# Kernel optimization log

Measured on AMD Instinct MI355X. Metric: run time of the kernel, lower is better.

Reference implementation:

```python
import jax, jax.numpy as jnp
import numpy as np

D_MODEL = 1024
HIDDEN = 4096
N_EXPERTS = 8
TOP_K = 2


def setup_inputs() -> dict:
    key = jax.random.key(0)
    ks = jax.random.split(key, 7)
    x = jax.random.normal(ks[0], (4, 2048, D_MODEL), dtype=jnp.float32)
    s = 0.02
    Wg = jax.random.normal(ks[1], (D_MODEL, N_EXPERTS), dtype=jnp.float32) * s
    bg = jnp.zeros((N_EXPERTS,), dtype=jnp.float32)
    W1 = jax.random.normal(ks[2], (N_EXPERTS, D_MODEL, HIDDEN), dtype=jnp.float32) * s
    b1 = jnp.zeros((N_EXPERTS, HIDDEN), dtype=jnp.float32)
    W2 = jax.random.normal(ks[3], (N_EXPERTS, HIDDEN, D_MODEL), dtype=jnp.float32) * s
    b2 = jnp.zeros((N_EXPERTS, D_MODEL), dtype=jnp.float32)
    return {"x": x, "Wg": Wg, "bg": bg, "W1": W1, "b1": b1, "W2": W2, "b2": b2}


def reference(x, Wg, bg, W1, b1, W2, b2):
    B, T, D = x.shape
    xf = x.reshape(-1, D)                      # (N, D)
    N = xf.shape[0]

    # --- top-k gate ---
    logits = xf @ Wg + bg                      # (N, E)
    all_probs = jax.nn.softmax(logits, axis=-1)
    topk_logits, topk_idx = jax.lax.top_k(logits, TOP_K)   # (N, k)
    topk_gates = jax.nn.softmax(topk_logits, axis=-1)      # (N, k), sums to 1

    # scatter gates into dense (N, E) masks (matches torch scatter_add_)
    rows = jnp.arange(N)[:, None]
    gate_mask = jnp.zeros((N, N_EXPERTS), dtype=xf.dtype).at[rows, topk_idx].add(topk_gates)
    dispatch_mask = jnp.zeros((N, N_EXPERTS), dtype=xf.dtype).at[rows, topk_idx].add(1.0)

    # --- experts: dense batched form; unselected tokens have gate 0 so math matches ---
    h = jnp.einsum('nd,edh->neh', xf, W1) + b1             # (N, E, H)
    h = jax.nn.relu(h)
    y = jnp.einsum('neh,ehd->ned', h, W2) + b2             # (N, E, D)
    out = jnp.einsum('ned,ne->nd', y, gate_mask)           # weighted combine
    outputs = out.reshape(B, T, D)

    # --- load-balance loss + metadata ---
    tokens_per_expert = (dispatch_mask > 0).sum(axis=0)
    assignment_fraction = gate_mask.sum(axis=0) / N
    expected_prob = all_probs.mean(axis=0)
    load_balance_loss = (expected_prob * assignment_fraction).sum() * N_EXPERTS

    return (outputs, load_balance_loss, tokens_per_expert, expected_prob, assignment_fraction)
```

## Files before the change

kernel.cpp:

```cpp
#include <hip/hip_runtime.h>
#include <stdint.h>

#define D_MODEL 1024
#define HID     4096
#define NE      8
#define NTOK    8192
#define NSLOT   (NTOK*2)
#define TM      128
#define MAX_RB  136
#define MPAD    (MAX_RB*TM)
#define HHALF   2048
#define GATE_BLOCKS 32

typedef unsigned short u16;
typedef __attribute__((ext_vector_type(8))) __bf16 bf16x8;
typedef __attribute__((ext_vector_type(4))) float  f32x4;

__device__ __forceinline__ u16 f2bu(float f){
  uint32_t u = __builtin_bit_cast(uint32_t, f);
  uint32_t r = (u + 0x7FFFu + ((u >> 16) & 1u)) >> 16;
  return (u16)r;
}

__device__ __forceinline__ void gload16(const u16* src, u16* lds){
  __builtin_amdgcn_global_load_lds((const __attribute__((address_space(1))) void*)src,
                                   (__attribute__((address_space(3))) void*)lds, 16, 0, 0);
}

__device__ __forceinline__ int xcd_swz(int w, int nwg){
  int q = nwg >> 3;
  return (w & 7) * q + (w >> 3);
}

__global__ __launch_bounds__(256) void xcvt_kernel(const float* __restrict__ x, u16* __restrict__ x16){
  size_t i = (size_t)blockIdx.x*256 + threadIdx.x;
  const float4* p = (const float4*)(x + i*8);
  float4 a = p[0], b = p[1];
  u16 o[8] = {f2bu(a.x),f2bu(a.y),f2bu(a.z),f2bu(a.w),f2bu(b.x),f2bu(b.y),f2bu(b.z),f2bu(b.w)};
  *(int4*)(x16 + i*8) = *(int4*)o;
}

__global__ __launch_bounds__(256) void transpose_cvt(const float* __restrict__ in,
                                                     u16* __restrict__ out, int R, int C)
{
  __shared__ float tile[32][33];
  int e = blockIdx.z;
  int r0 = blockIdx.y * 32, c0 = blockIdx.x * 32;
  const float* src = in + (size_t)e * R * C;
  u16* dst = out + (size_t)e * R * C;
  int tx = threadIdx.x, ty = threadIdx.y;
#pragma unroll
  for (int i = 0; i < 4; i++){
    int r = r0 + ty + i*8;
    tile[ty + i*8][tx] = src[(size_t)r * C + c0 + tx];
  }
  __syncthreads();
#pragma unroll
  for (int i = 0; i < 4; i++){
    int c = c0 + ty + i*8;
    dst[(size_t)c * R + r0 + tx] = f2bu(tile[tx][ty + i*8]);
  }
}

__global__ __launch_bounds__(256) void gate_kernel(
    const float* __restrict__ x, const float* __restrict__ Wg, const float* __restrict__ bg,
    int* __restrict__ topk, float* __restrict__ gates,
    float* __restrict__ part_probs, float* __restrict__ part_assign, int* __restrict__ part_cnt)
{
  __shared__ float sp[256][8];
  __shared__ float sa[256][8];
  __shared__ int   sc[256][8];
  int t = threadIdx.x;
  int n = blockIdx.x * 256 + t;
  float lg[8];
#pragma unroll
  for (int e = 0; e < 8; e++) lg[e] = bg[e];
  const float4* xr = (const float4*)(x + (size_t)n * D_MODEL);
  for (int j = 0; j < D_MODEL/4; j++){
    float4 v = xr[j];
    const float* wr = Wg + (size_t)j * 32;
#pragma unroll
    for (int e = 0; e < 8; e++)
      lg[e] += v.x*wr[e] + v.y*wr[8+e] + v.z*wr[16+e] + v.w*wr[24+e];
  }
  float m = lg[0];
#pragma unroll
  for (int e = 1; e < 8; e++) m = fmaxf(m, lg[e]);
  float p[8]; float s = 0.f;
#pragma unroll
  for (int e = 0; e < 8; e++){ p[e] = expf(lg[e]-m); s += p[e]; }
  float inv = 1.f / s;
  int bi = 0; float best = lg[0];
#pragma unroll
  for (int e = 1; e < 8; e++) if (lg[e] > best){ best = lg[e]; bi = e; }
  int bi2 = 0; float best2 = -3.0e38f;
#pragma unroll
  for (int e = 0; e < 8; e++) if (e != bi && lg[e] > best2){ best2 = lg[e]; bi2 = e; }
  float t1 = expf(best2 - best);
  float g0 = 1.f / (1.f + t1);
  float g1 = t1 / (1.f + t1);
  topk[2*n] = bi;  topk[2*n+1] = bi2;
  gates[2*n] = g0; gates[2*n+1] = g1;
#pragma unroll
  for (int e = 0; e < 8; e++){
    sp[t][e] = p[e] * inv;
    sa[t][e] = (e == bi) ? g0 : ((e == bi2) ? g1 : 0.f);
    sc[t][e] = (e == bi || e == bi2) ? 1 : 0;
  }
  __syncthreads();
  if (t < 8){
    float s2 = 0.f; for (int i = 0; i < 256; i++) s2 += sp[i][t];
    part_probs[blockIdx.x*8 + t] = s2;
  } else if (t < 16){
    int e = t - 8; float s2 = 0.f; for (int i = 0; i < 256; i++) s2 += sa[i][e];
    part_assign[blockIdx.x*8 + e] = s2;
  } else if (t < 24){
    int e = t - 16; int c = 0; for (int i = 0; i < 256; i++) c += sc[i][e];
    part_cnt[blockIdx.x*8 + e] = c;
  }
}

__global__ __launch_bounds__(256) void scan_kernel(const int* __restrict__ part_cnt,
                                                   int* __restrict__ counts,
                                                   int* __restrict__ padded_off,
                                                   int* __restrict__ cursor,
                                                   int* __restrict__ block_expert,
                                                   int* __restrict__ routed)
{
  __shared__ int off[NE+1];
  int t = threadIdx.x;
  if (t == 0){
    int o = 0; off[0] = 0;
    for (int e = 0; e < NE; e++){
      int c = 0;
      for (int b = 0; b < GATE_BLOCKS; b++) c += part_cnt[b*8 + e];
      counts[e] = c;
      o += ((c + TM - 1) / TM) * TM;
      off[e+1] = o;
    }
    for (int e = 0; e <= NE; e++) padded_off[e] = off[e];
  }
  __syncthreads();
  if (t < NE) cursor[t] = 0;
  for (int rb = t; rb < MAX_RB; rb += 256){
    int e = -1;
    int r = rb * TM;
    for (int j = 0; j < NE; j++)
      if (r >= off[j] && r < off[j+1]) e = j;
    block_expert[rb] = e;
  }
  for (int i = t; i < MPAD; i += 256) routed[i] = -1;
}

__global__ __launch_bounds__(256) void place_kernel(const int* __restrict__ topk,
                                                    const int* __restrict__ padded_off,
                                                    int* __restrict__ cursor,
                                                    int* __restrict__ routed)
{
  int s = blockIdx.x * 256 + threadIdx.x;
  int e = topk[s];
  int pos = padded_off[e] + atomicAdd(&cursor[e], 1);
  routed[pos] = s;
}

__global__ __launch_bounds__(256) void gemm1_kernel(
    const u16* __restrict__ x16, const u16* __restrict__ w1t, const float* __restrict__ b1,
    const int* __restrict__ routed, const int* __restrict__ block_expert,
    u16* __restrict__ h, int half)
{
  int l = xcd_swz(blockIdx.x, gridDim.x);
  int rb = l >> 4, cb = l & 15;
  int e = block_expert[rb];
  if (e < 0) return;
  __shared__ __align__(16) u16 Al[2][128][32];
  __shared__ __align__(16) u16 Bl[2][128][32];
  int t = threadIdx.x;
  int lane = t & 63, wid = t >> 6;

  int srow0 = wid*32 + (lane >> 2);
  int srow1 = srow0 + 16;
  int sch = (lane & 3) * 8;

  int slot0 = routed[rb*TM + srow0];
  int slot1 = routed[rb*TM + srow1];
  int tok0 = slot0 >= 0 ? (slot0 >> 1) : 0;
  int tok1 = slot1 >= 0 ? (slot1 >> 1) : 0;
  const u16* srcA0 = x16 + (size_t)tok0 * D_MODEL + sch;
  const u16* srcA1 = x16 + (size_t)tok1 * D_MODEL + sch;
  const u16* wb = w1t + ((size_t)e*HID + (size_t)half*HHALF + (size_t)cb*128) * D_MODEL + sch;
  const u16* srcB0 = wb + (size_t)srow0 * D_MODEL;
  const u16* srcB1 = wb + (size_t)srow1 * D_MODEL;

  int wr = wid >> 1, wc = wid & 1;
  int fr = lane & 15, fk = lane >> 4;
  f32x4 acc[4][4];
#pragma unroll
  for (int i = 0; i < 4; i++)
#pragma unroll
    for (int j = 0; j < 4; j++) acc[i][j] = (f32x4){0.f,0.f,0.f,0.f};

#define STAGE1(bi, kk) do{ \
    gload16(srcA0 + (kk), &Al[bi][wid*32][0]); \
    gload16(srcA1 + (kk), &Al[bi][wid*32+16][0]); \
    gload16(srcB0 + (kk), &Bl[bi][wid*32][0]); \
    gload16(srcB1 + (kk), &Bl[bi][wid*32+16][0]); } while(0)

#define COMPUTE1(bi) do{ \
    bf16x8 af[4], bf[4]; \
    _Pragma("unroll") \
    for (int mm = 0; mm < 4; mm++) af[mm] = *(const bf16x8*)(&Al[bi][wr*64 + mm*16 + fr][fk*8]); \
    _Pragma("unroll") \
    for (int nn = 0; nn < 4; nn++) bf[nn] = *(const bf16x8*)(&Bl[bi][wc*64 + nn*16 + fr][fk*8]); \
    _Pragma("unroll") \
    for (int mm = 0; mm < 4; mm++) \
      _Pragma("unroll") \
      for (int nn = 0; nn < 4; nn++) \
        acc[mm][nn] = __builtin_amdgcn_mfma_f32_16x16x32_bf16(af[mm], bf[nn], acc[mm][nn], 0, 0, 0); } while(0)

  STAGE1(0, 0);
  __syncthreads();
  for (int k = 0; k < D_MODEL; k += 64){
    STAGE1(1, k + 32);
    COMPUTE1(0);
    __syncthreads();
    if (k + 64 < D_MODEL) STAGE1(0, k + 64);
    COMPUTE1(1);
    __syncthreads();
  }

  int r4 = fk * 4;
#pragma unroll
  for (int nn = 0; nn < 4; nn++){
    int ct = wc*64 + nn*16 + fr;
    float bias = b1[(size_t)e*HID + (size_t)half*HHALF + cb*128 + ct];
#pragma unroll
    for (int mm = 0; mm < 4; mm++){
#pragma unroll
      for (int r = 0; r < 4; r++){
        int rt = wr*64 + mm*16 + r4 + r;
        float v = acc[mm][nn][r] + bias;
        v = v > 0.f ? v : 0.f;
        h[(size_t)(rb*TM + rt) * HHALF + cb*128 + ct] = f2bu(v);
      }
    }
  }
#undef STAGE1
#undef COMPUTE1
}

__global__ __launch_bounds__(256) void gemm2_kernel(
    const u16* __restrict__ h, const u16* __restrict__ w2t,
    const int* __restrict__ routed, const int* __restrict__ block_expert,
    const float* __restrict__ gates, float* __restrict__ y, int half)
{
  int l = xcd_swz(blockIdx.x, gridDim.x);
  int rb = l >> 3, cb = l & 7;
  int e = block_expert[rb];
  if (e < 0) return;
  __shared__ __align__(16) u16 Al[2][128][32];
  __shared__ __align__(16) u16 Bl[2][128][32];
  __shared__ int   rslot[128];
  __shared__ float rgate[128];
  int t = threadIdx.x;
  int lane = t & 63, wid = t >> 6;
  if (t < 128){
    int s = routed[rb*TM + t];
    rslot[t] = s;
    rgate[t] = (s >= 0) ? gates[s] : 0.f;
  }

  int srow0 = wid*32 + (lane >> 2);
  int srow1 = srow0 + 16;
  int sch = (lane & 3) * 8;
  const u16* srcA0 = h + (size_t)(rb*TM + srow0) * HHALF + sch;
  const u16* srcA1 = h + (size_t)(rb*TM + srow1) * HHALF + sch;
  const u16* wb = w2t + ((size_t)e*D_MODEL + (size_t)cb*128) * HID + (size_t)half*HHALF + sch;
  const u16* srcB0 = wb + (size_t)srow0 * HID;
  const u16* srcB1 = wb + (size_t)srow1 * HID;

  int wr = wid >> 1, wc = wid & 1;
  int fr = lane & 15, fk = lane >> 4;
  f32x4 acc[4][4];
#pragma unroll
  for (int i = 0; i < 4; i++)
#pragma unroll
    for (int j = 0; j < 4; j++) acc[i][j] = (f32x4){0.f,0.f,0.f,0.f};

#define STAGE2(bi, kk) do{ \
    gload16(srcA0 + (kk), &Al[bi][wid*32][0]); \
    gload16(srcA1 + (kk), &Al[bi][wid*32+16][0]); \
    gload16(srcB0 + (kk), &Bl[bi][wid*32][0]); \
    gload16(srcB1 + (kk), &Bl[bi][wid*32+16][0]); } while(0)

#define COMPUTE2(bi) do{ \
    bf16x8 af[4], bf[4]; \
    _Pragma("unroll") \
    for (int mm = 0; mm < 4; mm++) af[mm] = *(const bf16x8*)(&Al[bi][wr*64 + mm*16 + fr][fk*8]); \
    _Pragma("unroll") \
    for (int nn = 0; nn < 4; nn++) bf[nn] = *(const bf16x8*)(&Bl[bi][wc*64 + nn*16 + fr][fk*8]); \
    _Pragma("unroll") \
    for (int mm = 0; mm < 4; mm++) \
      _Pragma("unroll") \
      for (int nn = 0; nn < 4; nn++) \
        acc[mm][nn] = __builtin_amdgcn_mfma_f32_16x16x32_bf16(af[mm], bf[nn], acc[mm][nn], 0, 0, 0); } while(0)

  STAGE2(0, 0);
  __syncthreads();
  for (int k = 0; k < HHALF; k += 64){
    STAGE2(1, k + 32);
    COMPUTE2(0);
    __syncthreads();
    if (k + 64 < HHALF) STAGE2(0, k + 64);
    COMPUTE2(1);
    __syncthreads();
  }

  int r4 = fk * 4;
#pragma unroll
  for (int mm = 0; mm < 4; mm++){
#pragma unroll
    for (int r = 0; r < 4; r++){
      int rt = wr*64 + mm*16 + r4 + r;
      int slot = rslot[rt];
      if (slot < 0) continue;
      float g = rgate[rt];
#pragma unroll
      for (int nn = 0; nn < 4; nn++){
        int ct = wc*64 + nn*16 + fr;
        size_t idx = (size_t)slot * D_MODEL + cb*128 + ct;
        float val = g * acc[mm][nn][r];
        if (half == 0) y[idx] = val;
        else           y[idx] += val;
      }
    }
  }
#undef STAGE2
#undef COMPUTE2
}

__global__ __launch_bounds__(256) void combine_kernel(
    const float* __restrict__ y, const int* __restrict__ topk, const float* __restrict__ gates,
    const float* __restrict__ b2, float* __restrict__ out)
{
  int i = blockIdx.x * 256 + threadIdx.x;
  int n = i >> 8;
  int d = (i & 255) * 4;
  float4 a  = *(const float4*)(y + (size_t)(2*n)   * D_MODEL + d);
  float4 b  = *(const float4*)(y + (size_t)(2*n+1) * D_MODEL + d);
  int e0 = topk[2*n], e1 = topk[2*n+1];
  float g0 = gates[2*n], g1 = gates[2*n+1];
  float4 c0 = *(const float4*)(b2 + (size_t)e0 * D_MODEL + d);
  float4 c1 = *(const float4*)(b2 + (size_t)e1 * D_MODEL + d);
  float4 o;
  o.x = a.x + b.x + g0*c0.x + g1*c1.x;
  o.y = a.y + b.y + g0*c0.y + g1*c1.y;
  o.z = a.z + b.z + g0*c0.z + g1*c1.z;
  o.w = a.w + b.w + g0*c0.w + g1*c1.w;
  *(float4*)(out + (size_t)n * D_MODEL + d) = o;
}

__global__ void finalize_kernel(const float* __restrict__ part_probs,
                                const float* __restrict__ part_assign,
                                const int* __restrict__ counts,
                                float* __restrict__ out_tail)
{
  __shared__ float ep[8], af[8];
  int t = threadIdx.x;
  if (t < 8){
    float s = 0.f;
    for (int b = 0; b < GATE_BLOCKS; b++) s += part_probs[b*8 + t];
    ep[t] = s / (float)NTOK;
  } else if (t < 16){
    int e = t - 8; float s = 0.f;
    for (int b = 0; b < GATE_BLOCKS; b++) s += part_assign[b*8 + e];
    af[e] = s / (float)NTOK;
  }
  __syncthreads();
  if (t == 0){
    float loss = 0.f;
    for (int e = 0; e < 8; e++) loss += ep[e] * af[e];
    out_tail[0] = loss * (float)NE;
  }
  if (t < 8){
    out_tail[1 + t]  = (float)counts[t];
    out_tail[9 + t]  = ep[t];
    out_tail[17 + t] = af[t];
  }
}

extern "C" void kernel_launch(void* const* d_in, const int* in_sizes, int n_in,
                              void* d_out, int out_size, void* d_ws, size_t ws_size,
                              hipStream_t stream)
{
  const float* x  = (const float*)d_in[0];
  const float* Wg = (const float*)d_in[1];
  const float* bg = (const float*)d_in[2];
  const float* W1 = (const float*)d_in[3];
  const float* b1 = (const float*)d_in[4];
  const float* W2 = (const float*)d_in[5];
  const float* b2 = (const float*)d_in[6];
  float* out = (float*)d_out;

  char* ws = (char*)d_ws;
  size_t o = 0;
  auto alloc = [&](size_t bytes) -> char* {
    char* p = ws + o; o = (o + bytes + 255) & ~(size_t)255; return p;
  };
  int*   topk        = (int*)   alloc((size_t)NSLOT*4);
  float* gates       = (float*) alloc((size_t)NSLOT*4);
  int*   counts      = (int*)   alloc(NE*4);
  int*   padded_off  = (int*)   alloc((NE+1)*4);
  int*   cursor      = (int*)   alloc(NE*4);
  int*   block_exp   = (int*)   alloc(MAX_RB*4);
  int*   routed      = (int*)   alloc((size_t)MPAD*4);
  float* part_probs  = (float*) alloc(GATE_BLOCKS*8*4);
  float* part_assign = (float*) alloc(GATE_BLOCKS*8*4);
  int*   part_cnt    = (int*)   alloc(GATE_BLOCKS*8*4);
  u16*   x16         = (u16*)   alloc((size_t)NTOK*D_MODEL*2);
  u16*   w1t         = (u16*)   alloc((size_t)NE*HID*D_MODEL*2);
  u16*   w2t         = (u16*)   alloc((size_t)NE*HID*D_MODEL*2);
  u16*   hbuf        = (u16*)   alloc((size_t)MPAD*HHALF*2);
  float* ybuf        = (float*) alloc((size_t)NSLOT*D_MODEL*4);
  (void)ws_size; (void)in_sizes; (void)n_in; (void)out_size;

  transpose_cvt<<<dim3(HID/32, D_MODEL/32, NE), dim3(32,8), 0, stream>>>(W1, w1t, D_MODEL, HID);
  transpose_cvt<<<dim3(D_MODEL/32, HID/32, NE), dim3(32,8), 0, stream>>>(W2, w2t, HID, D_MODEL);
  xcvt_kernel<<<(NTOK*D_MODEL)/(256*8), 256, 0, stream>>>(x, x16);
  gate_kernel<<<GATE_BLOCKS, 256, 0, stream>>>(x, Wg, bg, topk, gates, part_probs, part_assign, part_cnt);
  scan_kernel<<<1, 256, 0, stream>>>(part_cnt, counts, padded_off, cursor, block_exp, routed);
  place_kernel<<<NSLOT/256, 256, 0, stream>>>(topk, padded_off, cursor, routed);
  for (int half = 0; half < 2; half++){
    gemm1_kernel<<<16*MAX_RB, 256, 0, stream>>>(x16, w1t, b1, routed, block_exp, hbuf, half);
    gemm2_kernel<<<8*MAX_RB, 256, 0, stream>>>(hbuf, w2t, routed, block_exp, gates, ybuf, half);
  }
  combine_kernel<<<NTOK, 256, 0, stream>>>(ybuf, topk, gates, b2, out);
  finalize_kernel<<<1, 64, 0, stream>>>(part_probs, part_assign, counts, out + (size_t)NTOK*D_MODEL);
}
```

Measured before the change: 754.7 us.

## Triple-buffer expert GEMM K-loop with explicit vmcnt waits and occupancy hint

Both expert GEMM kernels move from a double-buffered LDS loop, where each __syncthreads drains all outstanding global-to-LDS loads, to a three-stage ring. The new loop uses explicit s_waitcnt vmcnt counts, so two future K-slices stay in flight while the current one is computed. It also adds a launch_bounds minimum of 3 blocks per CU. The aim is to hide global load latency behind MFMA work, at the cost of 50% more LDS per block and tighter register limits.

```diff
diff --git a/kernel.cpp b/kernel.cpp
--- a/kernel.cpp
+++ b/kernel.cpp
@@ -31,6 +31,12 @@
   int q = nwg >> 3;
   return (w & 7) * q + (w >> 3);
 }
+
+#define WAITV(n) do{ asm volatile("s_waitcnt vmcnt(" #n ")" ::: "memory"); \
+                     __builtin_amdgcn_sched_barrier(0); }while(0)
+#define BARX()   do{ __builtin_amdgcn_sched_barrier(0); \
+                     __builtin_amdgcn_s_barrier(); \
+                     __builtin_amdgcn_sched_barrier(0); }while(0)
 
 __global__ __launch_bounds__(256) void xcvt_kernel(const float* __restrict__ x, u16* __restrict__ x16){
   size_t i = (size_t)blockIdx.x*256 + threadIdx.x;
@@ -163,7 +169,7 @@
   routed[pos] = s;
 }
 
-__global__ __launch_bounds__(256) void gemm1_kernel(
+__global__ __launch_bounds__(256, 3) void gemm1_kernel(
     const u16* __restrict__ x16, const u16* __restrict__ w1t, const float* __restrict__ b1,
     const int* __restrict__ routed, const int* __restrict__ block_expert,
     u16* __restrict__ h, int half)
@@ -172,24 +178,25 @@
   int rb = l >> 4, cb = l & 15;
   int e = block_expert[rb];
   if (e < 0) return;
-  __shared__ __align__(16) u16 Al[2][128][32];
-  __shared__ __align__(16) u16 Bl[2][128][32];
+  __shared__ __align__(16) u16 Al[3][128][32];
+  __shared__ __align__(16) u16 Bl[3][128][32];
+  u16* AF = &Al[0][0][0];
+  u16* BF = &Bl[0][0][0];
   int t = threadIdx.x;
   int lane = t & 63, wid = t >> 6;
 
   int srow0 = wid*32 + (lane >> 2);
-  int srow1 = srow0 + 16;
   int sch = (lane & 3) * 8;
 
   int slot0 = routed[rb*TM + srow0];
-  int slot1 = routed[rb*TM + srow1];
+  int slot1 = routed[rb*TM + srow0 + 16];
   int tok0 = slot0 >= 0 ? (slot0 >> 1) : 0;
   int tok1 = slot1 >= 0 ? (slot1 >> 1) : 0;
   const u16* srcA0 = x16 + (size_t)tok0 * D_MODEL + sch;
   const u16* srcA1 = x16 + (size_t)tok1 * D_MODEL + sch;
   const u16* wb = w1t + ((size_t)e*HID + (size_t)half*HHALF + (size_t)cb*128) * D_MODEL + sch;
   const u16* srcB0 = wb + (size_t)srow0 * D_MODEL;
-  const u16* srcB1 = wb + (size_t)srow1 * D_MODEL;
+  const u16* srcB1 = wb + (size_t)(srow0 + 16) * D_MODEL;
 
   int wr = wid >> 1, wc = wid & 1;
   int fr = lane & 15, fk = lane >> 4;
@@ -199,34 +206,38 @@
 #pragma unroll
     for (int j = 0; j < 4; j++) acc[i][j] = (f32x4){0.f,0.f,0.f,0.f};
 
-#define STAGE1(bi, kk) do{ \
-    gload16(srcA0 + (kk), &Al[bi][wid*32][0]); \
-    gload16(srcA1 + (kk), &Al[bi][wid*32+16][0]); \
-    gload16(srcB0 + (kk), &Bl[bi][wid*32][0]); \
-    gload16(srcB1 + (kk), &Bl[bi][wid*32+16][0]); } while(0)
-
-#define COMPUTE1(bi) do{ \
+#define STG1(bo, kk) do{ \
+    gload16(srcA0 + (kk), AF + (bo) + wid*1024); \
+    gload16(srcA1 + (kk), AF + (bo) + wid*1024 + 512); \
+    gload16(srcB0 + (kk), BF + (bo) + wid*1024); \
+    gload16(srcB1 + (kk), BF + (bo) + wid*1024 + 512); } while(0)
+
+#define CMP1(bo) do{ \
     bf16x8 af[4], bf[4]; \
     _Pragma("unroll") \
-    for (int mm = 0; mm < 4; mm++) af[mm] = *(const bf16x8*)(&Al[bi][wr*64 + mm*16 + fr][fk*8]); \
-    _Pragma("unroll") \
-    for (int nn = 0; nn < 4; nn++) bf[nn] = *(const bf16x8*)(&Bl[bi][wc*64 + nn*16 + fr][fk*8]); \
+    for (int mm = 0; mm < 4; mm++) af[mm] = *(const bf16x8*)(AF + (bo) + (wr*64 + mm*16 + fr)*32 + fk*8); \
+    _Pragma("unroll") \
+    for (int nn = 0; nn < 4; nn++) bf[nn] = *(const bf16x8*)(BF + (bo) + (wc*64 + nn*16 + fr)*32 + fk*8); \
     _Pragma("unroll") \
     for (int mm = 0; mm < 4; mm++) \
       _Pragma("unroll") \
       for (int nn = 0; nn < 4; nn++) \
         acc[mm][nn] = __builtin_amdgcn_mfma_f32_16x16x32_bf16(af[mm], bf[nn], acc[mm][nn], 0, 0, 0); } while(0)
 
-  STAGE1(0, 0);
-  __syncthreads();
-  for (int k = 0; k < D_MODEL; k += 64){
-    STAGE1(1, k + 32);
-    COMPUTE1(0);
-    __syncthreads();
-    if (k + 64 < D_MODEL) STAGE1(0, k + 64);
-    COMPUTE1(1);
-    __syncthreads();
-  }
+  const int nk = D_MODEL/32;
+  STG1(0, 0); STG1(4096, 32); STG1(8192, 64);
+  int bo = 0;
+  for (int i = 0; i < nk - 2; i++){
+    WAITV(8);
+    BARX();
+    CMP1(bo);
+    BARX();
+    if (i < nk - 3) STG1(bo, (i+3)*32);
+    bo = (bo == 8192) ? 0 : bo + 4096;
+  }
+  WAITV(4); BARX(); CMP1(bo); BARX();
+  bo = (bo == 8192) ? 0 : bo + 4096;
+  WAITV(0); BARX(); CMP1(bo);
 
   int r4 = fk * 4;
 #pragma unroll
@@ -244,11 +255,11 @@
       }
     }
   }
-#undef STAGE1
-#undef COMPUTE1
-}
-
-__global__ __launch_bounds__(256) void gemm2_kernel(
+#undef STG1
+#undef CMP1
+}
+
+__global__ __launch_bounds__(256, 3) void gemm2_kernel(
     const u16* __restrict__ h, const u16* __restrict__ w2t,
     const int* __restrict__ routed, const int* __restrict__ block_expert,
     const float* __restrict__ gates, float* __restrict__ y, int half)
@@ -257,10 +268,12 @@
   int rb = l >> 3, cb = l & 7;
   int e = block_expert[rb];
   if (e < 0) return;
-  __shared__ __align__(16) u16 Al[2][128][32];
-  __shared__ __align__(16) u16 Bl[2][128][32];
+  __shared__ __align__(16) u16 Al[3][128][32];
+  __shared__ __align__(16) u16 Bl[3][128][32];
   __shared__ int   rslot[128];
   __shared__ float rgate[128];
+  u16* AF = &Al[0][0][0];
+  u16* BF = &Bl[0][0][0];
   int t = threadIdx.x;
   int lane = t & 63, wid = t >> 6;
   if (t < 128){
@@ -270,13 +283,12 @@
   }
 
   int srow0 = wid*32 + (lane >> 2);
-  int srow1 = srow0 + 16;
   int sch = (lane & 3) * 8;
   const u16* srcA0 = h + (size_t)(rb*TM + srow0) * HHALF + sch;
-  const u16* srcA1 = h + (size_t)(rb*TM + srow1) * HHALF + sch;
+  const u16* srcA1 = h + (size_t)(rb*TM + srow0 + 16) * HHALF + sch;
   const u16* wb = w2t + ((size_t)e*D_MODEL + (size_t)cb*128) * HID + (size_t)half*HHALF + sch;
   const u16* srcB0 = wb + (size_t)srow0 * HID;
-  const u16* srcB1 = wb + (size_t)srow1 * HID;
+  const u16* srcB1 = wb + (size_t)(srow0 + 16) * HID;
 
   int wr = wid >> 1, wc = wid & 1;
   int fr = lane & 15, fk = lane >> 4;
@@ -286,34 +298,38 @@
 #pragma unroll
     for (int j = 0; j < 4; j++) acc[i][j] = (f32x4){0.f,0.f,0.f,0.f};
 
-#define STAGE2(bi, kk) do{ \
-    gload16(srcA0 + (kk), &Al[bi][wid*32][0]); \
-    gload16(srcA1 + (kk), &Al[bi][wid*32+16][0]); \
-    gload16(srcB0 + (kk), &Bl[bi][wid*32][0]); \
-    gload16(srcB1 + (kk), &Bl[bi][wid*32+16][0]); } while(0)
-
-#define COMPUTE2(bi) do{ \
+#define STG2(bo, kk) do{ \
+    gload16(srcA0 + (kk), AF + (bo) + wid*1024); \
+    gload16(srcA1 + (kk), AF + (bo) + wid*1024 + 512); \
+    gload16(srcB0 + (kk), BF + (bo) + wid*1024); \
+    gload16(srcB1 + (kk), BF + (bo) + wid*1024 + 512); } while(0)
+
+#define CMP2(bo) do{ \
     bf16x8 af[4], bf[4]; \
     _Pragma("unroll") \
-    for (int mm = 0; mm < 4; mm++) af[mm] = *(const bf16x8*)(&Al[bi][wr*64 + mm*16 + fr][fk*8]); \
-    _Pragma("unroll") \
-    for (int nn = 0; nn < 4; nn++) bf[nn] = *(const bf16x8*)(&Bl[bi][wc*64 + nn*16 + fr][fk*8]); \
+    for (int mm = 0; mm < 4; mm++) af[mm] = *(const bf16x8*)(AF + (bo) + (wr*64 + mm*16 + fr)*32 + fk*8); \
+    _Pragma("unroll") \
+    for (int nn = 0; nn < 4; nn++) bf[nn] = *(const bf16x8*)(BF + (bo) + (wc*64 + nn*16 + fr)*32 + fk*8); \
     _Pragma("unroll") \
     for (int mm = 0; mm < 4; mm++) \
       _Pragma("unroll") \
       for (int nn = 0; nn < 4; nn++) \
         acc[mm][nn] = __builtin_amdgcn_mfma_f32_16x16x32_bf16(af[mm], bf[nn], acc[mm][nn], 0, 0, 0); } while(0)
 
-  STAGE2(0, 0);
-  __syncthreads();
-  for (int k = 0; k < HHALF; k += 64){
-    STAGE2(1, k + 32);
-    COMPUTE2(0);
-    __syncthreads();
-    if (k + 64 < HHALF) STAGE2(0, k + 64);
-    COMPUTE2(1);
-    __syncthreads();
-  }
+  const int nk = HHALF/32;
+  STG2(0, 0); STG2(4096, 32); STG2(8192, 64);
+  int bo = 0;
+  for (int i = 0; i < nk - 2; i++){
+    WAITV(8);
+    BARX();
+    CMP2(bo);
+    BARX();
+    if (i < nk - 3) STG2(bo, (i+3)*32);
+    bo = (bo == 8192) ? 0 : bo + 4096;
+  }
+  WAITV(4); BARX(); CMP2(bo); BARX();
+  bo = (bo == 8192) ? 0 : bo + 4096;
+  WAITV(0); BARX(); CMP2(bo);
 
   int r4 = fk * 4;
 #pragma unroll
@@ -334,8 +350,8 @@
       }
     }
   }
-#undef STAGE2
-#undef COMPUTE2
+#undef STG2
+#undef CMP2
 }
 
 __global__ __launch_bounds__(256) void combine_kernel(
```

New measurement: 688.4 us. -8.8%, faster.
